# Kernel tuning notes

Hardware: AMD Instinct MI355X
Metric: run time of the kernel (lower is better)

Reference implementation:

```python
import jax, jax.numpy as jnp
import numpy as np

B, C, H, W = 32, 256, 32, 32
HEADS, DH = 8, 32          # MHA9: num_heads=8, dim_head=32, total_dim=256
TOT = HEADS * DH


def setup_inputs() -> dict:
    key = jax.random.key(0)
    ks = jax.random.split(key, 10)
    s = 0.02
    return {
        "x": jax.random.normal(ks[0], (B, C, H, W), dtype=jnp.float32),
        "Wq": jax.random.normal(ks[1], (TOT, C), dtype=jnp.float32) * s,
        "bq": jnp.zeros((TOT,), dtype=jnp.float32),
        "Wk": jax.random.normal(ks[2], (TOT, C), dtype=jnp.float32) * s,
        "bk": jnp.zeros((TOT,), dtype=jnp.float32),
        "Wv": jax.random.normal(ks[3], (TOT, C), dtype=jnp.float32) * s,
        "bv": jnp.zeros((TOT,), dtype=jnp.float32),
        "Wo": jax.random.normal(ks[4], (C, TOT), dtype=jnp.float32) * s,
        "bo": jnp.zeros((C,), dtype=jnp.float32),
        "gamma": jnp.zeros((1,), dtype=jnp.float32),
    }


def reference(x, Wq, bq, Wk, bk, Wv, bv, Wo, bo, gamma):
    b, c, h, w = x.shape
    S = h * w

    def proj(Wt, bt):
        # 1x1 conv == channel matmul; reshape to (B, heads, S, dh)
        y = jnp.einsum('oc,bchw->bohw', Wt, x) + bt[None, :, None, None]
        return y.reshape(b, HEADS, DH, S).transpose(0, 1, 3, 2)

    q = proj(Wq, bq)
    k = proj(Wk, bk)
    v = proj(Wv, bv)

    scale = 1.0 / jnp.sqrt(jnp.asarray(DH, dtype=x.dtype))
    scores = jnp.einsum('bhsd,bhtd->bhst', q, k) * scale  # [B,h,S,S] full matrix
    weights = jax.nn.softmax(scores, axis=-1)
    o = jnp.einsum('bhst,bhtd->bhsd', weights, v)          # [B,h,S,dh]
    o = o.transpose(0, 1, 3, 2).reshape(b, TOT, h, w)
    o = jnp.einsum('oc,bchw->bohw', Wo, o) + bo[None, :, None, None]
    x_ = gamma * o + x   # inner residual of MultiHeadAttention
    return x + x_        # outer residual of MulAttontion
```

## Files before the change

kernel.cpp:

```cpp
#include <hip/hip_runtime.h>
#include <stdint.h>

typedef unsigned short u16;
typedef unsigned int   u32;
typedef __attribute__((ext_vector_type(8))) short bf16x8;
typedef __attribute__((ext_vector_type(4))) short bf16x4;
typedef __attribute__((ext_vector_type(4))) float f32x4;
typedef __attribute__((ext_vector_type(16))) float f32x16;

#define NT ((size_t)8388608)

__device__ __forceinline__ float bf2f(u16 u) {
  union { float f; u32 i; } v; v.i = ((u32)u) << 16; return v.f;
}
__device__ __forceinline__ u16 f2bf(float f) {
  union { float f; u32 i; } v; v.f = f;
  u32 r = (v.i + 0x7fffu + ((v.i >> 16) & 1u)) >> 16;
  return (u16)r;
}
__device__ __forceinline__ u32 fbits(float f) {
  union { float f; u32 i; } v; v.f = f; return v.i;
}
__device__ __forceinline__ int detect_bf16(const u32* __restrict__ xd) {
  u32 w = xd[threadIdx.x & 63];
  u32 e = (w >> 8) & 0x7fu;
  unsigned long long m = __ballot((e >= 0x38u) && (e <= 0x41u));
  return __popcll(m) > 32;
}
__device__ __forceinline__ void gld16(const void* g, void* l) {
  __builtin_amdgcn_global_load_lds((const __attribute__((address_space(1))) u32*)g,
                                   (__attribute__((address_space(3))) u32*)l, 16, 0, 0);
}

__global__ void __launch_bounds__(256) prologue_kernel(const void* __restrict__ xin,
                                                       u16* __restrict__ xT,
                                                       const void* __restrict__ W0, const void* __restrict__ W1,
                                                       const void* __restrict__ W2, const void* __restrict__ b0,
                                                       const void* __restrict__ b1, const void* __restrict__ b2,
                                                       u16* __restrict__ wdst, float* __restrict__ bdst,
                                                       const void* __restrict__ Wo, const void* __restrict__ bo,
                                                       const void* __restrict__ gm, u16* __restrict__ wodst,
                                                       float* __restrict__ bodst) {
  const int blk = blockIdx.x;
  const int tid = threadIdx.x;
  const int isbf = detect_bf16((const u32*)xin);
  if (blk < 2048) {
    const int s0 = (blk & 15) * 64, c0 = ((blk >> 4) & 3) * 64, b = blk >> 6;
    __shared__ u16 T[64][72];
    if (isbf) {
      const u16* xp = (const u16*)xin;
      for (int t = tid; t < 512; t += 256) {
        int r = t >> 3, off = (t & 7) * 8;
        *(uint4*)&T[r][off] = *(const uint4*)(xp + ((size_t)(b * 256 + c0 + r)) * 1024 + s0 + off);
      }
    } else {
      const float* xp = (const float*)xin;
      for (int t = tid; t < 512; t += 256) {
        int r = t >> 3, off = (t & 7) * 8;
        const float* s = xp + ((size_t)(b * 256 + c0 + r)) * 1024 + s0 + off;
        const float4 a = *(const float4*)s;
        const float4 c = *(const float4*)(s + 4);
        T[r][off + 0] = f2bf(a.x); T[r][off + 1] = f2bf(a.y);
        T[r][off + 2] = f2bf(a.z); T[r][off + 3] = f2bf(a.w);
        T[r][off + 4] = f2bf(c.x); T[r][off + 5] = f2bf(c.y);
        T[r][off + 6] = f2bf(c.z); T[r][off + 7] = f2bf(c.w);
      }
    }
    __syncthreads();
    for (int t = tid; t < 512; t += 256) {
      int r = t >> 3, off = (t & 7) * 8;
      union { u16 h[8]; uint4 v; } pk;
#pragma unroll
      for (int u = 0; u < 8; u++) pk.h[u] = T[off + u][r];
      *(uint4*)(xT + ((size_t)(b * 1024 + s0 + r)) * 256 + c0 + off) = pk.v;
    }
  } else if (blk < 2240) {
    const int g = blk - 2048;
    const int which = g >> 6, bk = g & 63;
    const void* Ws = which == 0 ? W0 : which == 1 ? W1 : W2;
    const void* bs = which == 0 ? b0 : which == 1 ? b1 : b2;
    const int idx = bk * 1024 + tid * 4;
    u16* dst = wdst + which * 65536 + idx;
    if (isbf) {
      *(ushort4*)dst = *(const ushort4*)((const u16*)Ws + idx);
    } else {
      const float4 sv = *(const float4*)((const float*)Ws + idx);
      ushort4 o; o.x = f2bf(sv.x); o.y = f2bf(sv.y); o.z = f2bf(sv.z); o.w = f2bf(sv.w);
      *(ushort4*)dst = o;
    }
    if (bk == 0) {
      bdst[which * 256 + tid] = isbf ? bf2f(((const u16*)bs)[tid]) : ((const float*)bs)[tid];
    }
  } else {
    const int g = blk - 2240;
    const int idx = g * 1024 + tid * 4;
    if (isbf) {
      *(ushort4*)(wodst + idx) = *(const ushort4*)((const u16*)Wo + idx);
    } else {
      const float4 sv = *(const float4*)((const float*)Wo + idx);
      ushort4 o; o.x = f2bf(sv.x); o.y = f2bf(sv.y); o.z = f2bf(sv.z); o.w = f2bf(sv.w);
      *(ushort4*)(wodst + idx) = o;
    }
    if (g == 0) {
      bodst[tid] = isbf ? bf2f(((const u16*)bo)[tid]) : ((const float*)bo)[tid];
      if (tid == 0) bodst[256] = isbf ? bf2f(((const u16*)gm)[0]) : ((const float*)gm)[0];
    }
  }
}

__global__ void __launch_bounds__(256) prep_o(const void* __restrict__ Wo, const void* __restrict__ bo,
                                              const void* __restrict__ gm, u16* __restrict__ wdst,
                                              float* __restrict__ bdst, const u32* __restrict__ xdet) {
  const int isbf = detect_bf16(xdet);
  const int idx = blockIdx.x * 1024 + threadIdx.x * 4;
  if (isbf) {
    *(ushort4*)(wdst + idx) = *(const ushort4*)((const u16*)Wo + idx);
  } else {
    const float4 sv = *(const float4*)((const float*)Wo + idx);
    ushort4 o; o.x = f2bf(sv.x); o.y = f2bf(sv.y); o.z = f2bf(sv.z); o.w = f2bf(sv.w);
    *(ushort4*)(wdst + idx) = o;
  }
  if (blockIdx.x == 0) {
    int t = threadIdx.x;
    bdst[t] = isbf ? bf2f(((const u16*)bo)[t]) : ((const float*)bo)[t];
    if (t == 0) bdst[256] = isbf ? bf2f(((const u16*)gm)[0]) : ((const float*)gm)[0];
  }
}

__global__ void __launch_bounds__(256) qkv_gemm(const u16* __restrict__ xT,
                                                const u16* __restrict__ Wall,
                                                const float* __restrict__ ball,
                                                u16* __restrict__ Qb, u16* __restrict__ Kb,
                                                u16* __restrict__ Vb) {
  const int z = blockIdx.z, b = z / 3, which = z - b * 3;
  const int tid = threadIdx.x, lane = tid & 63, wave = tid >> 6;
  const int quad = lane >> 4, l16 = lane & 15;
  const int wm = wave >> 1, wn = wave & 1;
  const u16* xb = xT + (size_t)b * 262144;
  const u16* W = Wall + which * 65536;
  const int m0 = blockIdx.y * 128;
  const int n0 = blockIdx.x * 128;

  __shared__ u16 Ash[8192], Bsh[8192];
  f32x4 acc[4][4];
#pragma unroll
  for (int i = 0; i < 4; i++)
#pragma unroll
    for (int j = 0; j < 4; j++) acc[i][j] = (f32x4){0.f, 0.f, 0.f, 0.f};

  const int srow = lane >> 3;
  const int sgc = (lane & 7) ^ (srow & 7);
  for (int k0 = 0; k0 < 256; k0 += 64) {
    __syncthreads();
#pragma unroll
    for (int p = 0; p < 4; p++) {
      const int row = p * 32 + wave * 8;
      gld16(W  + (size_t)(m0 + row + srow) * 256 + k0 + sgc * 8, &Ash[row * 64 + lane * 8]);
      gld16(xb + (size_t)(n0 + row + srow) * 256 + k0 + sgc * 8, &Bsh[row * 64 + lane * 8]);
    }
    __syncthreads();
#pragma unroll
    for (int kk = 0; kk < 2; kk++) {
      bf16x8 av[4], bv[4];
      const int rg = (kk * 4 + quad) ^ (l16 & 7);
#pragma unroll
      for (int i = 0; i < 4; i++) av[i] = *(const bf16x8*)&Ash[(wm * 64 + i * 16 + l16) * 64 + rg * 8];
#pragma unroll
      for (int j = 0; j < 4; j++) bv[j] = *(const bf16x8*)&Bsh[(wn * 64 + j * 16 + l16) * 64 + rg * 8];
#pragma unroll
      for (int i = 0; i < 4; i++)
#pragma unroll
        for (int j = 0; j < 4; j++)
          acc[i][j] = __builtin_amdgcn_mfma_f32_16x16x32_bf16(av[i], bv[j], acc[i][j], 0, 0, 0);
    }
  }

  const float* bias = ball + which * 256;
  const float scale = (which == 0) ? 0.25503486f : 1.0f;
#pragma unroll
  for (int i = 0; i < 4; i++) {
#pragma unroll
    for (int j = 0; j < 4; j++) {
      const int mb = m0 + wm * 64 + i * 16 + quad * 4;
      const int n = n0 + wn * 64 + j * 16 + l16;
      if (which < 2) {
        u16* D = (which ? Kb : Qb) + (size_t)b * 262144;
        ushort4 st;
        st.x = f2bf((acc[i][j][0] + bias[mb + 0]) * scale);
        st.y = f2bf((acc[i][j][1] + bias[mb + 1]) * scale);
        st.z = f2bf((acc[i][j][2] + bias[mb + 2]) * scale);
        st.w = f2bf((acc[i][j][3] + bias[mb + 3]) * scale);
        *(ushort4*)(D + (size_t)(mb >> 5) * 32768 + (size_t)n * 32 + (mb & 31)) = st;
      } else {
        u16* D = Vb + (size_t)b * 262144;
#pragma unroll
        for (int r = 0; r < 4; r++) {
          const int m = mb + r;
          D[(size_t)m * 1024 + n] = f2bf(acc[i][j][r] + bias[m]);
        }
      }
    }
  }
}

__global__ void __launch_bounds__(512) attn_kernel(const u16* __restrict__ Q,
                                                   const u16* __restrict__ K,
                                                   const u16* __restrict__ V,
                                                   u16* __restrict__ O) {
  const int blk = blockIdx.x;
  const int qc = blk >> 8, bh = blk & 255;
  const int b = bh >> 3, h = bh & 7;
  const int tid = threadIdx.x, wave = tid >> 6, lane = tid & 63;
  const int hi = lane >> 5, l32 = lane & 31;
  __shared__ __align__(16) u16 Ksh[2][128 * 32];
  __shared__ __align__(16) u16 Vsh[2][32 * 128];
  const u16* Qg = Q + (size_t)b * 262144 + (size_t)h * 32768;
  const u16* Kg = K + (size_t)b * 262144 + (size_t)h * 32768;
  const u16* Vg = V + (size_t)b * 262144 + (size_t)h * 32768;
  const int qw = qc * 256 + wave * 32;

  bf16x8 qf[2];
#pragma unroll
  for (int ks = 0; ks < 2; ks++)
    qf[ks] = *(const bf16x8*)(Qg + (size_t)(qw + l32) * 32 + ks * 16 + hi * 8);

  const int Gg = wave * 64 + lane;
  const int th = Gg >> 3;
  const int uu = (Gg & 7) ^ (th & 7);
  const u16* ksrc = Kg + (size_t)(th * 2 + (uu >> 2)) * 32 + (uu & 3) * 8;
  u16* kdst0 = &Ksh[0][Gg * 8];
  u16* kdst1 = &Ksh[1][Gg * 8];
  const int vd = tid >> 4;
  const u16* vsrc = Vg + (size_t)vd * 1024 + ((tid & 15) ^ (vd & 15)) * 8;
  u16* vdst0 = &Vsh[0][tid * 8];
  u16* vdst1 = &Vsh[1][tid * 8];

  const int kkey = (l32 >> 1) & 7;
  const int kb0 = (l32 >> 1) * 128 + (((((l32 & 1) << 2) | 0 | hi) ^ kkey) << 4);
  const int kb1 = (l32 >> 1) * 128 + (((((l32 & 1) << 2) | 2 | hi) ^ kkey) << 4);
  int vb[4];
#pragma unroll
  for (int tt = 0; tt < 4; tt++) vb[tt] = l32 * 256 + (((l32 & 12) ^ (tt << 2)) << 4);
  const int vm0 = ((l32 & 3) ^ hi) << 4;
  const int vm1 = ((l32 & 3) ^ (2 | hi)) << 4;

  f32x16 oacc;
#pragma unroll
  for (int r = 0; r < 16; r++) oacc[r] = 0.f;
  f32x16 zro;
#pragma unroll
  for (int r = 0; r < 16; r++) zro[r] = 0.f;
  float lsum = 0.f;

  gld16(ksrc, kdst0);
  gld16(vsrc, vdst0);
  __syncthreads();

#pragma unroll 1
  for (int kt = 0; kt < 8; kt++) {
    const int c = kt & 1;
    if (kt < 7) {
      gld16(ksrc + (size_t)(kt + 1) * 4096, c ? kdst0 : kdst1);
      gld16(vsrc + (kt + 1) * 128,          c ? vdst0 : vdst1);
    }
    const char* Kb = (const char*)&Ksh[c][0];
    const char* Vb = (const char*)&Vsh[c][0];
#pragma unroll
    for (int tt = 0; tt < 4; tt++) {
      const bf16x8 kf0 = *(const bf16x8*)(Kb + tt * 2048 + kb0);
      const bf16x8 kf1 = *(const bf16x8*)(Kb + tt * 2048 + kb1);
      const bf16x8 vf0 = *(const bf16x8*)(Vb + vb[tt] + vm0);
      const bf16x8 vf1 = *(const bf16x8*)(Vb + vb[tt] + vm1);
      __builtin_amdgcn_s_setprio(1);
      f32x16 sf = __builtin_amdgcn_mfma_f32_32x32x16_bf16(kf0, qf[0], zro, 0, 0, 0);
      sf = __builtin_amdgcn_mfma_f32_32x32x16_bf16(kf1, qf[1], sf, 0, 0, 0);
      __builtin_amdgcn_s_setprio(0);
      {
        const float p0 = __builtin_amdgcn_exp2f(sf[0]);
        const float p1 = __builtin_amdgcn_exp2f(sf[1]);
        const float p2 = __builtin_amdgcn_exp2f(sf[2]);
        const float p3 = __builtin_amdgcn_exp2f(sf[3]);
        const float p4 = __builtin_amdgcn_exp2f(sf[4]);
        const float p5 = __builtin_amdgcn_exp2f(sf[5]);
        const float p6 = __builtin_amdgcn_exp2f(sf[6]);
        const float p7 = __builtin_amdgcn_exp2f(sf[7]);
        lsum += ((p0 + p1) + (p2 + p3)) + ((p4 + p5) + (p6 + p7));
        u32 wa, wb, wc, wd;
        asm("v_cvt_pk_bf16_f32 %0, %1, %2" : "=v"(wa) : "v"(p0), "v"(p1));
        asm("v_cvt_pk_bf16_f32 %0, %1, %2" : "=v"(wb) : "v"(p2), "v"(p3));
        asm("v_cvt_pk_bf16_f32 %0, %1, %2" : "=v"(wc) : "v"(p4), "v"(p5));
        asm("v_cvt_pk_bf16_f32 %0, %1, %2" : "=v"(wd) : "v"(p6), "v"(p7));
#if __has_builtin(__builtin_amdgcn_permlane32_swap)
        auto s0 = __builtin_amdgcn_permlane32_swap((int)wc, (int)wa, false, false);
        auto s1 = __builtin_amdgcn_permlane32_swap((int)wd, (int)wb, false, false);
        union { int w[4]; bf16x8 v; } pk;
        pk.w[0] = s0[1]; pk.w[1] = s1[1]; pk.w[2] = s0[0]; pk.w[3] = s1[0];
#else
        const u32 xa = __shfl_xor((int)wa, 32), xb = __shfl_xor((int)wb, 32);
        const u32 xc = __shfl_xor((int)wc, 32), xd = __shfl_xor((int)wd, 32);
        union { u32 w[4]; bf16x8 v; } pk;
        pk.w[0] = hi ? xc : wa; pk.w[1] = hi ? xd : wb;
        pk.w[2] = hi ? wc : xa; pk.w[3] = hi ? wd : xb;
#endif
        __builtin_amdgcn_s_setprio(1);
        oacc = __builtin_amdgcn_mfma_f32_32x32x16_bf16(pk.v, vf0, oacc, 0, 0, 0);
        __builtin_amdgcn_s_setprio(0);
      }
      {
        const float p0 = __builtin_amdgcn_exp2f(sf[8]);
        const float p1 = __builtin_amdgcn_exp2f(sf[9]);
        const float p2 = __builtin_amdgcn_exp2f(sf[10]);
        const float p3 = __builtin_amdgcn_exp2f(sf[11]);
        const float p4 = __builtin_amdgcn_exp2f(sf[12]);
        const float p5 = __builtin_amdgcn_exp2f(sf[13]);
        const float p6 = __builtin_amdgcn_exp2f(sf[14]);
        const float p7 = __builtin_amdgcn_exp2f(sf[15]);
        lsum += ((p0 + p1) + (p2 + p3)) + ((p4 + p5) + (p6 + p7));
        u32 wa, wb, wc, wd;
        asm("v_cvt_pk_bf16_f32 %0, %1, %2" : "=v"(wa) : "v"(p0), "v"(p1));
        asm("v_cvt_pk_bf16_f32 %0, %1, %2" : "=v"(wb) : "v"(p2), "v"(p3));
        asm("v_cvt_pk_bf16_f32 %0, %1, %2" : "=v"(wc) : "v"(p4), "v"(p5));
        asm("v_cvt_pk_bf16_f32 %0, %1, %2" : "=v"(wd) : "v"(p6), "v"(p7));
#if __has_builtin(__builtin_amdgcn_permlane32_swap)
        auto s0 = __builtin_amdgcn_permlane32_swap((int)wc, (int)wa, false, false);
        auto s1 = __builtin_amdgcn_permlane32_swap((int)wd, (int)wb, false, false);
        union { int w[4]; bf16x8 v; } pk;
        pk.w[0] = s0[1]; pk.w[1] = s1[1]; pk.w[2] = s0[0]; pk.w[3] = s1[0];
#else
        const u32 xa = __shfl_xor((int)wa, 32), xb = __shfl_xor((int)wb, 32);
        const u32 xc = __shfl_xor((int)wc, 32), xd = __shfl_xor((int)wd, 32);
        union { u32 w[4]; bf16x8 v; } pk;
        pk.w[0] = hi ? xc : wa; pk.w[1] = hi ? xd : wb;
        pk.w[2] = hi ? wc : xa; pk.w[3] = hi ? wd : xb;
#endif
        __builtin_amdgcn_s_setprio(1);
        oacc = __builtin_amdgcn_mfma_f32_32x32x16_bf16(pk.v, vf1, oacc, 0, 0, 0);
        __builtin_amdgcn_s_setprio(0);
      }
    }
    if (kt < 7) __syncthreads();
  }

  lsum += __shfl_xor(lsum, 32);
  const float linv = 1.0f / lsum;
  u16* Og = O + (size_t)(b * 1024 + qw) * 256 + h * 32 + l32;
#pragma unroll
  for (int r = 0; r < 16; r++) {
    const int qo = (r & 3) + 8 * (r >> 2) + 4 * hi;
    const float li = __shfl(linv, qo);
    Og[(size_t)qo * 256] = f2bf(oacc[r] * li);
  }
}

__global__ void __launch_bounds__(256) out_gemm(const u16* __restrict__ WoB,
                                                const float* __restrict__ bg,
                                                const u16* __restrict__ Ob,
                                                const void* __restrict__ xin,
                                                void* __restrict__ outp,
                                                const u32* __restrict__ xdet) {
  const int b = blockIdx.z;
  const int m0 = blockIdx.x * 128;
  const int n0 = blockIdx.y * 64;
  const int tid = threadIdx.x, lane = tid & 63, wave = tid >> 6;
  const int quad = lane >> 4, l16 = lane & 15;
  const int wm = wave >> 1, wn = wave & 1;
  const int isbf = detect_bf16(xdet);
  const u16* Ab = Ob + (size_t)b * 262144;
  __shared__ u16 Ash[8192], Bsh[4096];
  f32x4 acc[4][2];
#pragma unroll
  for (int i = 0; i < 4; i++)
#pragma unroll
    for (int j = 0; j < 2; j++) acc[i][j] = (f32x4){0.f, 0.f, 0.f, 0.f};

  const int srow = lane >> 3;
  const int sgc = (lane & 7) ^ (srow & 7);
  for (int k0 = 0; k0 < 256; k0 += 64) {
    __syncthreads();
#pragma unroll
    for (int p = 0; p < 4; p++) {
      const int row = p * 32 + wave * 8;
      gld16(Ab + (size_t)(m0 + row + srow) * 256 + k0 + sgc * 8, &Ash[row * 64 + lane * 8]);
    }
#pragma unroll
    for (int p = 0; p < 2; p++) {
      const int row = p * 32 + wave * 8;
      gld16(WoB + (size_t)(n0 + row + srow) * 256 + k0 + sgc * 8, &Bsh[row * 64 + lane * 8]);
    }
    __syncthreads();
#pragma unroll
    for (int kk = 0; kk < 2; kk++) {
      bf16x8 av[4], bv[2];
      const int rg = (kk * 4 + quad) ^ (l16 & 7);
#pragma unroll
      for (int i = 0; i < 4; i++) av[i] = *(const bf16x8*)&Ash[(wm * 64 + i * 16 + l16) * 64 + rg * 8];
#pragma unroll
      for (int j = 0; j < 2; j++) bv[j] = *(const bf16x8*)&Bsh[(wn * 32 + j * 16 + l16) * 64 + rg * 8];
#pragma unroll
      for (int i = 0; i < 4; i++)
#pragma unroll
        for (int j = 0; j < 2; j++)
          acc[i][j] = __builtin_amdgcn_mfma_f32_16x16x32_bf16(av[i], bv[j], acc[i][j], 0, 0, 0);
    }
  }

  const float g = bg[256];
#pragma unroll
  for (int i = 0; i < 4; i++) {
#pragma unroll
    for (int j = 0; j < 2; j++) {
      const int mb = m0 + wm * 64 + i * 16 + quad * 4;
      const int n = n0 + wn * 32 + j * 16 + l16;
      const float bc = bg[n];
      const size_t gi = (size_t)b * 262144 + (size_t)n * 1024 + mb;
      if (isbf) {
        const ushort4 xv = *(const ushort4*)((const u16*)xin + gi);
        ushort4 st;
        st.x = f2bf(2.f * bf2f(xv.x) + g * (acc[i][j][0] + bc));
        st.y = f2bf(2.f * bf2f(xv.y) + g * (acc[i][j][1] + bc));
        st.z = f2bf(2.f * bf2f(xv.z) + g * (acc[i][j][2] + bc));
        st.w = f2bf(2.f * bf2f(xv.w) + g * (acc[i][j][3] + bc));
        *(ushort4*)((u16*)outp + gi) = st;
      } else {
        const float4 xv = *(const float4*)((const float*)xin + gi);
        float4 st;
        st.x = 2.f * xv.x + g * (acc[i][j][0] + bc);
        st.y = 2.f * xv.y + g * (acc[i][j][1] + bc);
        st.z = 2.f * xv.z + g * (acc[i][j][2] + bc);
        st.w = 2.f * xv.w + g * (acc[i][j][3] + bc);
        *(float4*)((float*)outp + gi) = st;
      }
    }
  }
}

extern "C" void kernel_launch(void* const* d_in, const int* in_sizes, int n_in,
                              void* d_out, int out_size, void* d_ws, size_t ws_size,
                              hipStream_t stream) {
  const void* x  = d_in[0];
  const void* Wq = d_in[1]; const void* bq = d_in[2];
  const void* Wk = d_in[3]; const void* bk = d_in[4];
  const void* Wv = d_in[5]; const void* bv = d_in[6];
  const void* Wo = d_in[7]; const void* bo = d_in[8];
  const void* gm = d_in[9];

  u16* ws = (u16*)d_ws;
  u16* xT = ws;
  u16* Qb = ws + NT;
  u16* Kb = ws + 2 * NT;
  u16* Vb = ws + 3 * NT;
  u16* Ob = xT;
  const u32* xdet = (const u32*)x;

  u16* WqkvB = (u16*)d_out;
  float* bqkvF = (float*)((u16*)d_out + 196608);

  const bool tail = ws_size >= (size_t)(4 * NT + 66048) * 2;
  u16* WoB = tail ? (ws + 4 * NT) : Qb;
  float* boF = tail ? (float*)(ws + 4 * NT + 65536) : (float*)(Qb + 65536);

  prologue_kernel<<<dim3(tail ? 2304 : 2240), 256, 0, stream>>>(
      x, xT, Wq, Wk, Wv, bq, bk, bv, WqkvB, bqkvF, Wo, bo, gm, WoB, boF);
  qkv_gemm<<<dim3(8, 2, 96), 256, 0, stream>>>(xT, WqkvB, bqkvF, Qb, Kb, Vb);
  attn_kernel<<<dim3(1024), 512, 0, stream>>>(Qb, Kb, Vb, Ob);
  if (!tail) prep_o<<<dim3(64), 256, 0, stream>>>(Wo, bo, gm, WoB, boF, xdet);
  out_gemm<<<dim3(8, 4, 32), 256, 0, stream>>>(WoB, boF, Ob, x, d_out, xdet);
}
```

Baseline: 191.7 us.

## Fuse x transpose and bf16 conversion into QKV GEMM B-tile loading

Removes the transpose of x from the prologue kernel. The QKV GEMM now reads x straight from its NCHW layout, converts it to bf16 in registers, and writes it transposed into a padded LDS tile using perm or pack instructions. This drops a full write and read of the transposed activation buffer and shrinks the prologue grid. In exchange, each of the three projection blocks (Q, K, V) re-reads and re-converts x, the B-tile global loads become synchronous register loads instead of async LDS loads, and LDS stores are now strided.

```diff
diff --git a/kernel.cpp b/kernel.cpp
--- a/kernel.cpp
+++ b/kernel.cpp
@@ -33,7 +33,6 @@
 }
 
 __global__ void __launch_bounds__(256) prologue_kernel(const void* __restrict__ xin,
-                                                       u16* __restrict__ xT,
                                                        const void* __restrict__ W0, const void* __restrict__ W1,
                                                        const void* __restrict__ W2, const void* __restrict__ b0,
                                                        const void* __restrict__ b1, const void* __restrict__ b2,
@@ -44,39 +43,8 @@
   const int blk = blockIdx.x;
   const int tid = threadIdx.x;
   const int isbf = detect_bf16((const u32*)xin);
-  if (blk < 2048) {
-    const int s0 = (blk & 15) * 64, c0 = ((blk >> 4) & 3) * 64, b = blk >> 6;
-    __shared__ u16 T[64][72];
-    if (isbf) {
-      const u16* xp = (const u16*)xin;
-      for (int t = tid; t < 512; t += 256) {
-        int r = t >> 3, off = (t & 7) * 8;
-        *(uint4*)&T[r][off] = *(const uint4*)(xp + ((size_t)(b * 256 + c0 + r)) * 1024 + s0 + off);
-      }
-    } else {
-      const float* xp = (const float*)xin;
-      for (int t = tid; t < 512; t += 256) {
-        int r = t >> 3, off = (t & 7) * 8;
-        const float* s = xp + ((size_t)(b * 256 + c0 + r)) * 1024 + s0 + off;
-        const float4 a = *(const float4*)s;
-        const float4 c = *(const float4*)(s + 4);
-        T[r][off + 0] = f2bf(a.x); T[r][off + 1] = f2bf(a.y);
-        T[r][off + 2] = f2bf(a.z); T[r][off + 3] = f2bf(a.w);
-        T[r][off + 4] = f2bf(c.x); T[r][off + 5] = f2bf(c.y);
-        T[r][off + 6] = f2bf(c.z); T[r][off + 7] = f2bf(c.w);
-      }
-    }
-    __syncthreads();
-    for (int t = tid; t < 512; t += 256) {
-      int r = t >> 3, off = (t & 7) * 8;
-      union { u16 h[8]; uint4 v; } pk;
-#pragma unroll
-      for (int u = 0; u < 8; u++) pk.h[u] = T[off + u][r];
-      *(uint4*)(xT + ((size_t)(b * 1024 + s0 + r)) * 256 + c0 + off) = pk.v;
-    }
-  } else if (blk < 2240) {
-    const int g = blk - 2048;
-    const int which = g >> 6, bk = g & 63;
+  if (blk < 192) {
+    const int which = blk >> 6, bk = blk & 63;
     const void* Ws = which == 0 ? W0 : which == 1 ? W1 : W2;
     const void* bs = which == 0 ? b0 : which == 1 ? b1 : b2;
     const int idx = bk * 1024 + tid * 4;
@@ -92,7 +60,7 @@
       bdst[which * 256 + tid] = isbf ? bf2f(((const u16*)bs)[tid]) : ((const float*)bs)[tid];
     }
   } else {
-    const int g = blk - 2240;
+    const int g = blk - 192;
     const int idx = g * 1024 + tid * 4;
     if (isbf) {
       *(ushort4*)(wodst + idx) = *(const ushort4*)((const u16*)Wo + idx);
@@ -127,7 +95,7 @@
   }
 }
 
-__global__ void __launch_bounds__(256) qkv_gemm(const u16* __restrict__ xT,
+__global__ void __launch_bounds__(256) qkv_gemm(const void* __restrict__ xin,
                                                 const u16* __restrict__ Wall,
                                                 const float* __restrict__ ball,
                                                 u16* __restrict__ Qb, u16* __restrict__ Kb,
@@ -136,12 +104,14 @@
   const int tid = threadIdx.x, lane = tid & 63, wave = tid >> 6;
   const int quad = lane >> 4, l16 = lane & 15;
   const int wm = wave >> 1, wn = wave & 1;
-  const u16* xb = xT + (size_t)b * 262144;
+  const int isbf = detect_bf16((const u32*)xin);
   const u16* W = Wall + which * 65536;
   const int m0 = blockIdx.y * 128;
   const int n0 = blockIdx.x * 128;
 
-  __shared__ u16 Ash[8192], Bsh[8192];
+  __shared__ u16 Ash[8192];
+  __shared__ __align__(16) u16 Bsh[128 * 72];
+  u32* B32 = (u32*)Bsh;
   f32x4 acc[4][4];
 #pragma unroll
   for (int i = 0; i < 4; i++)
@@ -150,13 +120,49 @@
 
   const int srow = lane >> 3;
   const int sgc = (lane & 7) ^ (srow & 7);
+  const int cp = tid & 31, sg = tid >> 5, si = sg * 16;
+
   for (int k0 = 0; k0 < 256; k0 += 64) {
+    float fa[16], fb[16];
+    uint4 ua[2], ub[2];
+    if (isbf) {
+      const u16* ra = (const u16*)xin + ((size_t)(b * 256 + k0 + 2 * cp)) * 1024 + n0 + si;
+      ua[0] = *(const uint4*)ra; ua[1] = *(const uint4*)(ra + 8);
+      ub[0] = *(const uint4*)(ra + 1024); ub[1] = *(const uint4*)(ra + 1032);
+    } else {
+      const float* ra = (const float*)xin + ((size_t)(b * 256 + k0 + 2 * cp)) * 1024 + n0 + si;
+      const float* rb = ra + 1024;
+#pragma unroll
+      for (int q = 0; q < 4; q++) {
+        const float4 va = ((const float4*)ra)[q];
+        const float4 vc = ((const float4*)rb)[q];
+        fa[q * 4 + 0] = va.x; fa[q * 4 + 1] = va.y; fa[q * 4 + 2] = va.z; fa[q * 4 + 3] = va.w;
+        fb[q * 4 + 0] = vc.x; fb[q * 4 + 1] = vc.y; fb[q * 4 + 2] = vc.z; fb[q * 4 + 3] = vc.w;
+      }
+    }
     __syncthreads();
+    if (isbf) {
+      const u32* au = (const u32*)ua;
+      const u32* bu = (const u32*)ub;
+#pragma unroll
+      for (int j = 0; j < 8; j++) {
+        const u32 lo = __builtin_amdgcn_perm(bu[j], au[j], 0x05040100u);
+        const u32 hi = __builtin_amdgcn_perm(bu[j], au[j], 0x07060302u);
+        B32[(si + 2 * j) * 36 + cp] = lo;
+        B32[(si + 2 * j + 1) * 36 + cp] = hi;
+      }
+    } else {
+#pragma unroll
+      for (int i = 0; i < 16; i++) {
+        u32 w;
+        asm("v_cvt_pk_bf16_f32 %0, %1, %2" : "=v"(w) : "v"(fa[i]), "v"(fb[i]));
+        B32[(si + i) * 36 + cp] = w;
+      }
+    }
 #pragma unroll
     for (int p = 0; p < 4; p++) {
       const int row = p * 32 + wave * 8;
-      gld16(W  + (size_t)(m0 + row + srow) * 256 + k0 + sgc * 8, &Ash[row * 64 + lane * 8]);
-      gld16(xb + (size_t)(n0 + row + srow) * 256 + k0 + sgc * 8, &Bsh[row * 64 + lane * 8]);
+      gld16(W + (size_t)(m0 + row + srow) * 256 + k0 + sgc * 8, &Ash[row * 64 + lane * 8]);
     }
     __syncthreads();
 #pragma unroll
@@ -166,7 +172,7 @@
 #pragma unroll
       for (int i = 0; i < 4; i++) av[i] = *(const bf16x8*)&Ash[(wm * 64 + i * 16 + l16) * 64 + rg * 8];
 #pragma unroll
-      for (int j = 0; j < 4; j++) bv[j] = *(const bf16x8*)&Bsh[(wn * 64 + j * 16 + l16) * 64 + rg * 8];
+      for (int j = 0; j < 4; j++) bv[j] = *(const bf16x8*)&Bsh[(wn * 64 + j * 16 + l16) * 72 + kk * 32 + quad * 8];
 #pragma unroll
       for (int i = 0; i < 4; i++)
 #pragma unroll
@@ -459,9 +465,9 @@
   u16* WoB = tail ? (ws + 4 * NT) : Qb;
   float* boF = tail ? (float*)(ws + 4 * NT + 65536) : (float*)(Qb + 65536);
 
-  prologue_kernel<<<dim3(tail ? 2304 : 2240), 256, 0, stream>>>(
-      x, xT, Wq, Wk, Wv, bq, bk, bv, WqkvB, bqkvF, Wo, bo, gm, WoB, boF);
-  qkv_gemm<<<dim3(8, 2, 96), 256, 0, stream>>>(xT, WqkvB, bqkvF, Qb, Kb, Vb);
+  prologue_kernel<<<dim3(tail ? 256 : 192), 256, 0, stream>>>(
+      x, Wq, Wk, Wv, bq, bk, bv, WqkvB, bqkvF, Wo, bo, gm, WoB, boF);
+  qkv_gemm<<<dim3(8, 2, 96), 256, 0, stream>>>(x, WqkvB, bqkvF, Qb, Kb, Vb);
   attn_kernel<<<dim3(1024), 512, 0, stream>>>(Qb, Kb, Vb, Ob);
   if (!tail) prep_o<<<dim3(64), 256, 0, stream>>>(Wo, bo, gm, WoB, boF, xdet);
   out_gemm<<<dim3(8, 4, 32), 256, 0, stream>>>(WoB, boF, Ob, x, d_out, xdet);
```

Measured after the change: 205.4 us. 1.07x slower.
